# Kernel tuning notes

Measured on AMD Instinct MI355X. Metric: run time of the kernel, lower is better.

The kernel has to match this reference:

```python
import jax, jax.numpy as jnp
import numpy as np

N, E, D_IN, D, D_OUT, L = 50000, 800000, 128, 256, 64, 3
TAU0 = 0.5
LN_EPS = 1e-5


def setup_inputs() -> dict:
    key = jax.random.key(0)
    ks = jax.random.split(key, 16)
    u01 = jax.random.uniform(ks[2], (L, 2, N, 2), minval=1e-6, maxval=1.0 - 1e-6)
    gumbel = -jnp.log(-jnp.log(u01))  # standard Gumbel(0,1) noise, one draw per layer per action net
    s = lambda k, shape, fan: jax.random.normal(k, shape) * np.float32(1.0 / np.sqrt(fan))
    return {
        'x': jax.random.normal(ks[0], (N, D_IN), dtype=jnp.float32),
        'edge_index': jax.random.randint(ks[1], (2, E), 0, N),
        'gumbel_noise': gumbel,
        'W_enc': s(ks[3], (D_IN, D), D_IN), 'b_enc': jnp.zeros((D,), jnp.float32),
        'W_root': s(ks[4], (L, D, D), D), 'W_agg': s(ks[5], (L, D, D), D), 'b_env': jnp.zeros((L, D), jnp.float32),
        'Wa_in_r': s(ks[6], (D, 2), D), 'Wa_in_a': s(ks[7], (D, 2), D), 'b_in': jnp.zeros((2,), jnp.float32),
        'Wa_out_r': s(ks[8], (D, 2), D), 'Wa_out_a': s(ks[9], (D, 2), D), 'b_out': jnp.zeros((2,), jnp.float32),
        'Wt_r': s(ks[10], (D, 1), D), 'Wt_a': s(ks[11], (D, 1), D), 'b_t': jnp.zeros((1,), jnp.float32),
        'ln_g': jnp.ones((D,), jnp.float32), 'ln_b': jnp.zeros((D,), jnp.float32),
        'W_dec': s(ks[12], (D, D_OUT), D), 'b_dec': jnp.zeros((D_OUT,), jnp.float32),
    }


def reference(x, edge_index, gumbel_noise, W_enc, b_enc, W_root, W_agg, b_env,
              Wa_in_r, Wa_in_a, b_in, Wa_out_r, Wa_out_a, b_out,
              Wt_r, Wt_a, b_t, ln_g, ln_b, W_dec, b_dec):
    n = x.shape[0]
    u, v = edge_index[0], edge_index[1]  # message flows v -> u (aggregate at u)

    def conv(h, Wr, Wa, b, ew=None):
        # GraphConv-style: root transform + sum-aggregated (optionally edge-weighted) neighbor transform
        msg = h[v] if ew is None else ew[:, None] * h[v]  # [E, D]
        agg = jax.ops.segment_sum(msg, u, num_segments=n)  # [N, D]
        return h @ Wr + agg @ Wa + b

    def layernorm(h):
        m = jnp.mean(h, axis=-1, keepdims=True)
        var = jnp.mean((h - m) ** 2, axis=-1, keepdims=True)
        return (h - m) * jax.lax.rsqrt(var + LN_EPS) * ln_g + ln_b

    def gumbel_hard(logits, g, temp):
        # hard gumbel-softmax with straight-through estimator, per-node temperature
        y = jax.nn.softmax((logits + g) / temp, axis=-1)
        hard = jax.nn.one_hot(jnp.argmax(y, axis=-1), 2, dtype=y.dtype)
        return hard + y - jax.lax.stop_gradient(y)

    # env encoder + (dropout=identity) + relu
    h = jax.nn.relu(x @ W_enc + b_enc)

    for l in range(W_root.shape[0]):
        h = layernorm(h)
        in_logits = conv(h, Wa_in_r, Wa_in_a, b_in)    # [N, 2]
        out_logits = conv(h, Wa_out_r, Wa_out_a, b_out)  # [N, 2]
        t = conv(h, Wt_r, Wt_a, b_t)                   # [N, 1]
        temp = 1.0 / (jax.nn.softplus(t) + TAU0)       # TempSoftPlus: per-node inverse temperature
        in_prob = gumbel_hard(in_logits, gumbel_noise[l, 0], temp)
        out_prob = gumbel_hard(out_logits, gumbel_noise[l, 1], temp)
        ew = in_prob[:, 0][u] * out_prob[:, 0][v]      # [E] gated edge weights
        h = jax.nn.relu(conv(h, W_root[l], W_agg[l], b_env[l], ew))

    h = layernorm(h)
    return h @ W_dec + b_dec
```

## Files before the change

### kernel.cpp

```cpp
#include <hip/hip_runtime.h>
#include <cstdint>

#define NN 50000
#define EE 800000
#define DIN 128
#define DD 256
#define DOUT 64
#define NLAYERS 3
#define LN_EPS 1e-5f
#define NB_SCAN ((NN + 255) / 256)

typedef __attribute__((ext_vector_type(8))) unsigned short us8;
typedef __attribute__((ext_vector_type(8))) short bs8;
typedef __attribute__((ext_vector_type(4))) float f4;

__device__ __forceinline__ float waveSum(float v) {
#pragma unroll
  for (int m = 1; m < 64; m <<= 1) v += __shfl_xor(v, m, 64);
  return v;
}

__device__ __forceinline__ void split3(float a, unsigned short& s1, unsigned short& s2,
                                       unsigned short& s3) {
  unsigned int b = __float_as_uint(a);
  s1 = (unsigned short)(b >> 16);
  float r1 = a - __uint_as_float(b & 0xffff0000u);
  unsigned int c = __float_as_uint(r1);
  s2 = (unsigned short)(c >> 16);
  float r2 = r1 - __uint_as_float(c & 0xffff0000u);
  s3 = (unsigned short)(__float_as_uint(r2) >> 16);
}

__device__ __forceinline__ void split8(float4 a, float4 b, us8& l1, us8& l2, us8& l3) {
  unsigned short s1, s2, s3;
  split3(a.x, s1, s2, s3); l1[0] = s1; l2[0] = s2; l3[0] = s3;
  split3(a.y, s1, s2, s3); l1[1] = s1; l2[1] = s2; l3[1] = s3;
  split3(a.z, s1, s2, s3); l1[2] = s1; l2[2] = s2; l3[2] = s3;
  split3(a.w, s1, s2, s3); l1[3] = s1; l2[3] = s2; l3[3] = s3;
  split3(b.x, s1, s2, s3); l1[4] = s1; l2[4] = s2; l3[4] = s3;
  split3(b.y, s1, s2, s3); l1[5] = s1; l2[5] = s2; l3[5] = s3;
  split3(b.z, s1, s2, s3); l1[6] = s1; l2[6] = s2; l3[6] = s3;
  split3(b.w, s1, s2, s3); l1[7] = s1; l2[7] = s2; l3[7] = s3;
}

__global__ __launch_bounds__(256) void k_encoder(const float* __restrict__ x,
                                                 const float* __restrict__ W,
                                                 const float* __restrict__ b,
                                                 float* __restrict__ h) {
  __shared__ float xs[8][DIN];
  const int tid = threadIdx.x;
  const int row0 = blockIdx.x * 8;
  {
    int idx = tid * 4;
    int r = idx >> 7, c = idx & 127;
    int row = row0 + r;
    float4 v = make_float4(0.f, 0.f, 0.f, 0.f);
    if (row < NN) v = *(const float4*)(x + (size_t)row * DIN + c);
    *(float4*)(&xs[r][c]) = v;
  }
  __syncthreads();
  float acc[8] = {0.f, 0.f, 0.f, 0.f, 0.f, 0.f, 0.f, 0.f};
  const int d = tid;
#pragma unroll 8
  for (int k = 0; k < DIN; ++k) {
    float wk = W[(size_t)k * DD + d];
#pragma unroll
    for (int r = 0; r < 8; ++r) acc[r] = fmaf(xs[r][k], wk, acc[r]);
  }
  float bb = b[d];
#pragma unroll
  for (int r = 0; r < 8; ++r) {
    int row = row0 + r;
    if (row < NN) h[(size_t)row * DD + d] = fmaxf(acc[r] + bb, 0.f);
  }
}

__global__ __launch_bounds__(256) void k_ln_scalars(
    const float* __restrict__ h, const float* __restrict__ ln_g, const float* __restrict__ ln_b,
    const float* __restrict__ Wir, const float* __restrict__ Wia,
    const float* __restrict__ Wor, const float* __restrict__ Woa,
    float* __restrict__ hn, float* __restrict__ SR, float* __restrict__ SA) {
  const int lane = threadIdx.x & 63;
  const int node = blockIdx.x * 4 + (threadIdx.x >> 6);
  if (node >= NN) return;
  const float4 hv = *(const float4*)(h + (size_t)node * DD + lane * 4);
  float m = waveSum(hv.x + hv.y + hv.z + hv.w) * (1.f / DD);
  float dx = hv.x - m, dy = hv.y - m, dz = hv.z - m, dw = hv.w - m;
  float var = waveSum(dx * dx + dy * dy + dz * dz + dw * dw) * (1.f / DD);
  float rs = 1.f / sqrtf(var + LN_EPS);
  const float4 g = *(const float4*)(ln_g + lane * 4);
  const float4 bb = *(const float4*)(ln_b + lane * 4);
  float4 o;
  o.x = fmaf(dx * rs, g.x, bb.x);
  o.y = fmaf(dy * rs, g.y, bb.y);
  o.z = fmaf(dz * rs, g.z, bb.z);
  o.w = fmaf(dw * rs, g.w, bb.w);
  *(float4*)(hn + (size_t)node * DD + lane * 4) = o;
  float p[8];
  const float4 a0 = *(const float4*)(Wir + 8 * lane);
  const float4 a1 = *(const float4*)(Wir + 8 * lane + 4);
  p[0] = o.x * a0.x + o.y * a0.z + o.z * a1.x + o.w * a1.z;
  p[1] = o.x * a0.y + o.y * a0.w + o.z * a1.y + o.w * a1.w;
  const float4 c0 = *(const float4*)(Wia + 8 * lane);
  const float4 c1 = *(const float4*)(Wia + 8 * lane + 4);
  p[2] = o.x * c0.x + o.y * c0.z + o.z * c1.x + o.w * c1.z;
  p[3] = o.x * c0.y + o.y * c0.w + o.z * c1.y + o.w * c1.w;
  const float4 e0 = *(const float4*)(Wor + 8 * lane);
  const float4 e1 = *(const float4*)(Wor + 8 * lane + 4);
  p[4] = o.x * e0.x + o.y * e0.z + o.z * e1.x + o.w * e1.z;
  p[5] = o.x * e0.y + o.y * e0.w + o.z * e1.y + o.w * e1.w;
  const float4 f0 = *(const float4*)(Woa + 8 * lane);
  const float4 f1 = *(const float4*)(Woa + 8 * lane + 4);
  p[6] = o.x * f0.x + o.y * f0.z + o.z * f1.x + o.w * f1.z;
  p[7] = o.x * f0.y + o.y * f0.w + o.z * f1.y + o.w * f1.w;
#pragma unroll
  for (int j = 0; j < 8; ++j) p[j] = waveSum(p[j]);
  if (lane == 0) {
    *(float4*)(SR + (size_t)node * 4) = make_float4(p[0], p[1], p[4], p[5]);
    *(float4*)(SA + (size_t)node * 4) = make_float4(p[2], p[3], p[6], p[7]);
  }
}

__global__ void k_zero_deg(int* __restrict__ deg) {
  int i = blockIdx.x * 256 + threadIdx.x;
  if (i < NN) deg[i] = 0;
}

__global__ void k_deg(const int* __restrict__ ei, int* __restrict__ deg) {
  int e = blockIdx.x * 256 + threadIdx.x;
  if (e < EE) atomicAdd(&deg[ei[e]], 1);
}

__global__ __launch_bounds__(256) void k_scan1(const int* __restrict__ deg,
                                               int* __restrict__ bsum) {
  __shared__ int sm[256];
  const int t = threadIdx.x;
  int i = blockIdx.x * 256 + t;
  sm[t] = (i < NN) ? deg[i] : 0;
  __syncthreads();
  for (int off = 128; off > 0; off >>= 1) {
    if (t < off) sm[t] += sm[t + off];
    __syncthreads();
  }
  if (t == 0) bsum[blockIdx.x] = sm[0];
}

__global__ __launch_bounds__(256) void k_scan2(const int* __restrict__ bsum,
                                               int* __restrict__ boff,
                                               int* __restrict__ rowptr) {
  __shared__ int sm[256];
  const int t = threadIdx.x;
  int v = (t < NB_SCAN) ? bsum[t] : 0;
  sm[t] = v;
  __syncthreads();
  for (int off = 1; off < 256; off <<= 1) {
    int x = (t >= off) ? sm[t - off] : 0;
    __syncthreads();
    sm[t] += x;
    __syncthreads();
  }
  if (t < NB_SCAN) boff[t] = sm[t] - v;
  if (t == 0) rowptr[NN] = sm[255];
}

__global__ __launch_bounds__(256) void k_scan3(const int* __restrict__ deg,
                                               const int* __restrict__ boff,
                                               int* __restrict__ rowptr,
                                               int* __restrict__ cursor) {
  __shared__ int sm[256];
  const int t = threadIdx.x;
  int i = blockIdx.x * 256 + t;
  int v = (i < NN) ? deg[i] : 0;
  sm[t] = v;
  __syncthreads();
  for (int off = 1; off < 256; off <<= 1) {
    int x = (t >= off) ? sm[t - off] : 0;
    __syncthreads();
    sm[t] += x;
    __syncthreads();
  }
  if (i < NN) {
    int r = boff[blockIdx.x] + sm[t] - v;
    rowptr[i] = r;
    cursor[i] = r;
  }
}

__global__ void k_fill(const int* __restrict__ ei, int* __restrict__ cursor,
                       int* __restrict__ csr_v) {
  int e = blockIdx.x * 256 + threadIdx.x;
  if (e >= EE) return;
  int u = ei[e], v = ei[EE + e];
  int slot = atomicAdd(&cursor[u], 1);
  csr_v[slot] = v;
}

__global__ void k_prep_w3(const float* __restrict__ Wr, const float* __restrict__ Wa, int l,
                          unsigned short* __restrict__ W1, unsigned short* __restrict__ W2,
                          unsigned short* __restrict__ W3) {
  int idx = blockIdx.x * 256 + threadIdx.x;
  if (idx >= DD * 2 * DD) return;
  int n = idx >> 9;
  int k = idx & 511;
  float w = (k < DD) ? Wr[((size_t)l * DD + k) * DD + n]
                     : Wa[((size_t)l * DD + (k - DD)) * DD + n];
  unsigned short s1, s2, s3;
  split3(w, s1, s2, s3);
  W1[idx] = s1; W2[idx] = s2; W3[idx] = s3;
}

__global__ __launch_bounds__(256) void k_gates_csr(
    const int* __restrict__ rowptr, const int* __restrict__ csr_v,
    const float* __restrict__ SR, const float* __restrict__ SA,
    const float* __restrict__ gn, const float* __restrict__ b_in,
    const float* __restrict__ b_out, unsigned char* __restrict__ gin,
    unsigned char* __restrict__ gout, int l) {
  int u = blockIdx.x * 256 + threadIdx.x;
  if (u >= NN) return;
  int beg = rowptr[u], end = rowptr[u + 1];
  float4 a = make_float4(0.f, 0.f, 0.f, 0.f);
  for (int j = beg; j < end; ++j) {
    int v = csr_v[j];
    float4 s = *(const float4*)(SA + (size_t)v * 4);
    a.x += s.x; a.y += s.y; a.z += s.z; a.w += s.w;
  }
  float4 r = *(const float4*)(SR + (size_t)u * 4);
  const float* gi = gn + ((size_t)(l * 2 + 0) * NN + u) * 2;
  const float* go = gn + ((size_t)(l * 2 + 1) * NN + u) * 2;
  float li0 = r.x + a.x + b_in[0] + gi[0];
  float li1 = r.y + a.y + b_in[1] + gi[1];
  gin[u] = (li0 >= li1) ? 1 : 0;
  float lo0 = r.z + a.z + b_out[0] + go[0];
  float lo1 = r.w + a.w + b_out[1] + go[1];
  gout[u] = (lo0 >= lo1) ? 1 : 0;
}

__global__ __launch_bounds__(256) void k_wagg_csr(
    const int* __restrict__ rowptr, const int* __restrict__ csr_v,
    const unsigned char* __restrict__ gin, const unsigned char* __restrict__ gout,
    const float* __restrict__ hn, float* __restrict__ agg) {
  const int lane = threadIdx.x & 63;
  const int u = blockIdx.x * 4 + (threadIdx.x >> 6);
  if (u >= NN) return;
  float4 acc = make_float4(0.f, 0.f, 0.f, 0.f);
  float4 acc2 = make_float4(0.f, 0.f, 0.f, 0.f);
  if (gin[u]) {
    int beg = rowptr[u], end = rowptr[u + 1];
    for (int j0 = beg; j0 < end; j0 += 64) {
      int rem = end - j0;
      int v = -1;
      if (lane < rem) v = csr_v[j0 + lane];
      int ok = (v >= 0) ? (int)gout[v] : 0;
      unsigned long long mask = __ballot(ok);
      while (mask) {
        int l0 = __builtin_ctzll(mask);
        mask &= mask - 1;
        int vv0 = __shfl(v, l0);
        const float4* p0 = (const float4*)(hn + (size_t)vv0 * DD + lane * 4);
        if (mask) {
          int l1 = __builtin_ctzll(mask);
          mask &= mask - 1;
          int vv1 = __shfl(v, l1);
          const float4* p1 = (const float4*)(hn + (size_t)vv1 * DD + lane * 4);
          float4 h0 = *p0;
          float4 h1 = *p1;
          acc.x += h0.x; acc.y += h0.y; acc.z += h0.z; acc.w += h0.w;
          acc2.x += h1.x; acc2.y += h1.y; acc2.z += h1.z; acc2.w += h1.w;
        } else {
          float4 h0 = *p0;
          acc.x += h0.x; acc.y += h0.y; acc.z += h0.z; acc.w += h0.w;
        }
      }
    }
    acc.x += acc2.x; acc.y += acc2.y; acc.z += acc2.z; acc.w += acc2.w;
  }
  *(float4*)(agg + (size_t)u * DD + lane * 4) = acc;
}

#define BM 128
#define BN 128
#define LDP 40

__global__ __launch_bounds__(256, 2) void k_conv_mfma(
    const float* __restrict__ A0,
    const float* __restrict__ A1,
    const unsigned short* __restrict__ B1, const unsigned short* __restrict__ B2,
    const unsigned short* __restrict__ B3,
    const float* __restrict__ bias, float* __restrict__ hout) {
  __shared__ unsigned short lA1[BM * LDP], lA2[BM * LDP], lA3[BM * LDP];
  __shared__ unsigned short lB1[BN * LDP], lB2[BN * LDP], lB3[BN * LDP];
  const int tid = threadIdx.x;
  const int j0 = blockIdx.x * BN;
  const int i0 = blockIdx.y * BM;
  const int lane = tid & 63, w = tid >> 6;
  const int wr = w >> 1, wc = w & 1;
  const int fr = lane & 15, fs = (lane >> 4) * 8;
  const int srow = tid >> 1, sc0 = (tid & 1) * 16;
  int ga = i0 + srow;
  if (ga >= NN) ga = NN - 1;
  const size_t aoff = (size_t)ga * DD;
  const size_t boff = (size_t)(j0 + srow) * (2 * DD);
  const f4 fz = {0.f, 0.f, 0.f, 0.f};
  f4 acc[4][4];
#pragma unroll
  for (int i = 0; i < 4; ++i)
#pragma unroll
    for (int j = 0; j < 4; ++j) acc[i][j] = fz;

  float4 fa0, fa1, fa2, fa3;
  us8 rb1a, rb1b, rb2a, rb2b, rb3a, rb3b;
  {
    const float* pa = A0 + aoff + sc0;
    fa0 = *(const float4*)(pa);      fa1 = *(const float4*)(pa + 4);
    fa2 = *(const float4*)(pa + 8);  fa3 = *(const float4*)(pa + 12);
    rb1a = *(const us8*)(B1 + boff + sc0); rb1b = *(const us8*)(B1 + boff + sc0 + 8);
    rb2a = *(const us8*)(B2 + boff + sc0); rb2b = *(const us8*)(B2 + boff + sc0 + 8);
    rb3a = *(const us8*)(B3 + boff + sc0); rb3b = *(const us8*)(B3 + boff + sc0 + 8);
  }
  for (int kt = 0; kt < 16; ++kt) {
    __syncthreads();
    {
      int o = srow * LDP + sc0;
      us8 x1, x2, x3, y1, y2, y3;
      split8(fa0, fa1, x1, x2, x3);
      split8(fa2, fa3, y1, y2, y3);
      *(us8*)&lA1[o] = x1; *(us8*)&lA1[o + 8] = y1;
      *(us8*)&lA2[o] = x2; *(us8*)&lA2[o + 8] = y2;
      *(us8*)&lA3[o] = x3; *(us8*)&lA3[o + 8] = y3;
      *(us8*)&lB1[o] = rb1a; *(us8*)&lB1[o + 8] = rb1b;
      *(us8*)&lB2[o] = rb2a; *(us8*)&lB2[o + 8] = rb2b;
      *(us8*)&lB3[o] = rb3a; *(us8*)&lB3[o + 8] = rb3b;
    }
    __syncthreads();
    if (kt < 15) {
      int kb = (kt + 1) * 32;
      const float* abase = (kb < DD) ? A0 : A1;
      int kk = kb & (DD - 1);
      const float* pa = abase + aoff + kk + sc0;
      fa0 = *(const float4*)(pa);      fa1 = *(const float4*)(pa + 4);
      fa2 = *(const float4*)(pa + 8);  fa3 = *(const float4*)(pa + 12);
      rb1a = *(const us8*)(B1 + boff + kb + sc0); rb1b = *(const us8*)(B1 + boff + kb + sc0 + 8);
      rb2a = *(const us8*)(B2 + boff + kb + sc0); rb2b = *(const us8*)(B2 + boff + kb + sc0 + 8);
      rb3a = *(const us8*)(B3 + boff + kb + sc0); rb3b = *(const us8*)(B3 + boff + kb + sc0 + 8);
    }
    bs8 a1[4], a2[4], a3[4];
#pragma unroll
    for (int mi = 0; mi < 4; ++mi) {
      int r = (wr * 64 + mi * 16 + fr) * LDP + fs;
      a1[mi] = *(const bs8*)&lA1[r];
      a2[mi] = *(const bs8*)&lA2[r];
      a3[mi] = *(const bs8*)&lA3[r];
    }
#pragma unroll
    for (int ni = 0; ni < 4; ++ni) {
      int c = (wc * 64 + ni * 16 + fr) * LDP + fs;
      bs8 b1 = *(const bs8*)&lB1[c];
      bs8 b2 = *(const bs8*)&lB2[c];
      bs8 b3 = *(const bs8*)&lB3[c];
#pragma unroll
      for (int mi = 0; mi < 4; ++mi) {
        acc[mi][ni] = __builtin_amdgcn_mfma_f32_16x16x32_bf16(a1[mi], b1, acc[mi][ni], 0, 0, 0);
        acc[mi][ni] = __builtin_amdgcn_mfma_f32_16x16x32_bf16(a1[mi], b2, acc[mi][ni], 0, 0, 0);
        acc[mi][ni] = __builtin_amdgcn_mfma_f32_16x16x32_bf16(a2[mi], b1, acc[mi][ni], 0, 0, 0);
        acc[mi][ni] = __builtin_amdgcn_mfma_f32_16x16x32_bf16(a1[mi], b3, acc[mi][ni], 0, 0, 0);
        acc[mi][ni] = __builtin_amdgcn_mfma_f32_16x16x32_bf16(a2[mi], b2, acc[mi][ni], 0, 0, 0);
        acc[mi][ni] = __builtin_amdgcn_mfma_f32_16x16x32_bf16(a3[mi], b1, acc[mi][ni], 0, 0, 0);
      }
    }
  }
#pragma unroll
  for (int ni = 0; ni < 4; ++ni) {
    int col = j0 + wc * 64 + ni * 16 + fr;
    float bv = bias[col];
#pragma unroll
    for (int mi = 0; mi < 4; ++mi) {
      int rbase = i0 + wr * 64 + mi * 16 + (lane >> 4) * 4;
#pragma unroll
      for (int r = 0; r < 4; ++r) {
        int row = rbase + r;
        if (row < NN) hout[(size_t)row * DD + col] = fmaxf(acc[mi][ni][r] + bv, 0.f);
      }
    }
  }
}

__global__ __launch_bounds__(256) void k_dec(const float* __restrict__ hn,
                                             const float* __restrict__ Wd, const float* __restrict__ bd,
                                             float* __restrict__ out) {
  __shared__ float As[64][33];
  __shared__ float Bs[32][65];
  const int tid = threadIdx.x;
  const int i0 = blockIdx.x * 64;
  const int tx = tid & 15, ty = tid >> 4;
  const int arow = tid >> 2, acol = (tid & 3) * 8;
  const int brow = tid >> 3, bcol = (tid & 7) * 8;
  float acc[4][4] = {{0.f}};
  for (int k0 = 0; k0 < DD; k0 += 32) {
    {
      int gr = i0 + arow;
      if (gr >= NN) gr = NN - 1;
      const float* src = hn + (size_t)gr * DD + k0 + acol;
      *(float4*)(&As[arow][acol]) = *(const float4*)(src);
      *(float4*)(&As[arow][acol + 4]) = *(const float4*)(src + 4);
    }
    {
      const float* src = Wd + (size_t)(k0 + brow) * DOUT + bcol;
      *(float4*)(&Bs[brow][bcol]) = *(const float4*)(src);
      *(float4*)(&Bs[brow][bcol + 4]) = *(const float4*)(src + 4);
    }
    __syncthreads();
#pragma unroll
    for (int kk = 0; kk < 32; ++kk) {
      float av[4], bv[4];
#pragma unroll
      for (int r = 0; r < 4; ++r) av[r] = As[ty * 4 + r][kk];
#pragma unroll
      for (int c = 0; c < 4; ++c) bv[c] = Bs[kk][tx * 4 + c];
#pragma unroll
      for (int r = 0; r < 4; ++r)
#pragma unroll
        for (int c = 0; c < 4; ++c) acc[r][c] = fmaf(av[r], bv[c], acc[r][c]);
    }
    __syncthreads();
  }
  const float4 bj = *(const float4*)(bd + tx * 4);
#pragma unroll
  for (int r = 0; r < 4; ++r) {
    int gr = i0 + ty * 4 + r;
    if (gr < NN) {
      float4 o;
      o.x = acc[r][0] + bj.x;
      o.y = acc[r][1] + bj.y;
      o.z = acc[r][2] + bj.z;
      o.w = acc[r][3] + bj.w;
      *(float4*)(out + (size_t)gr * DOUT + tx * 4) = o;
    }
  }
}

extern "C" void kernel_launch(void* const* d_in, const int* in_sizes, int n_in,
                              void* d_out, int out_size, void* d_ws, size_t ws_size,
                              hipStream_t stream) {
  const float* x = (const float*)d_in[0];
  const int* ei = (const int*)d_in[1];
  const float* gn = (const float*)d_in[2];
  const float* W_enc = (const float*)d_in[3];
  const float* b_enc = (const float*)d_in[4];
  const float* W_root = (const float*)d_in[5];
  const float* W_agg = (const float*)d_in[6];
  const float* b_env = (const float*)d_in[7];
  const float* Wa_in_r = (const float*)d_in[8];
  const float* Wa_in_a = (const float*)d_in[9];
  const float* b_in = (const float*)d_in[10];
  const float* Wa_out_r = (const float*)d_in[11];
  const float* Wa_out_a = (const float*)d_in[12];
  const float* b_out = (const float*)d_in[13];
  const float* ln_g = (const float*)d_in[17];
  const float* ln_b = (const float*)d_in[18];
  const float* W_dec = (const float*)d_in[19];
  const float* b_dec = (const float*)d_in[20];
  float* out = (float*)d_out;

  float* ws = (float*)d_ws;
  size_t off = 0;
  float* h = ws + off;    off += (size_t)NN * DD;
  float* hn = ws + off;   off += (size_t)NN * DD;
  float* agg = ws + off;  off += (size_t)NN * DD;
  float* SR = ws + off;   off += (size_t)NN * 4;
  float* SA = ws + off;   off += (size_t)NN * 4;
  int* rowptr = (int*)(ws + off); off += (size_t)NN + 4;
  int* csr_v = (int*)(ws + off);  off += (size_t)EE;
  unsigned char* gin = (unsigned char*)(ws + off);  off += (size_t)NN / 4;
  unsigned char* gout = (unsigned char*)(ws + off); off += (size_t)NN / 4;
  unsigned short* WT1 = (unsigned short*)(ws + off); off += (size_t)DD * 2 * DD / 2;
  unsigned short* WT2 = (unsigned short*)(ws + off); off += (size_t)DD * 2 * DD / 2;
  unsigned short* WT3 = (unsigned short*)(ws + off); off += (size_t)DD * 2 * DD / 2;
  if (ws_size < off * sizeof(float)) return;
  int* deg = (int*)SR;
  int* bsum = (int*)SR + NN;
  int* boff = (int*)SR + NN + 256;
  int* cursor = (int*)SA;

  k_zero_deg<<<(NN + 255) / 256, 256, 0, stream>>>(deg);
  k_deg<<<(EE + 255) / 256, 256, 0, stream>>>(ei, deg);
  k_scan1<<<NB_SCAN, 256, 0, stream>>>(deg, bsum);
  k_scan2<<<1, 256, 0, stream>>>(bsum, boff, rowptr);
  k_scan3<<<NB_SCAN, 256, 0, stream>>>(deg, boff, rowptr, cursor);
  k_fill<<<(EE + 255) / 256, 256, 0, stream>>>(ei, cursor, csr_v);

  k_encoder<<<(NN + 7) / 8, 256, 0, stream>>>(x, W_enc, b_enc, h);

  for (int l = 0; l < NLAYERS; ++l) {
    k_ln_scalars<<<(NN + 3) / 4, 256, 0, stream>>>(h, ln_g, ln_b, Wa_in_r, Wa_in_a,
                                                   Wa_out_r, Wa_out_a, hn, SR, SA);
    k_gates_csr<<<(NN + 255) / 256, 256, 0, stream>>>(rowptr, csr_v, SR, SA, gn,
                                                      b_in, b_out, gin, gout, l);
    k_wagg_csr<<<(NN + 3) / 4, 256, 0, stream>>>(rowptr, csr_v, gin, gout, hn, agg);
    k_prep_w3<<<(DD * 2 * DD + 255) / 256, 256, 0, stream>>>(W_root, W_agg, l, WT1, WT2, WT3);
    k_conv_mfma<<<dim3(2, (NN + BM - 1) / BM), 256, 0, stream>>>(
        hn, agg, WT1, WT2, WT3, b_env + (size_t)l * DD, h);
  }

  k_ln_scalars<<<(NN + 3) / 4, 256, 0, stream>>>(h, ln_g, ln_b, Wa_in_r, Wa_in_a,
                                                 Wa_out_r, Wa_out_a, hn, SR, SA);
  k_dec<<<(NN + 63) / 64, 256, 0, stream>>>(hn, W_dec, b_dec, out);
}
```

Measured before the change: 919.2 us.

## Switch GEMMs to 2-term fp16 split MFMA and route encoder/decoder through it

Replaces the 3-way bf16 split (6 MFMAs per tile step) with a 2-way fp16 hi/lo split using 3 MFMAs, which halves the tensor-core work and the shared-memory traffic of the conv GEMM. The kernel becomes a template that is also used for the encoder and decoder GEMMs, replacing their scalar FP32 kernels. Launch bounds rise to 4 blocks per CU, since less shared memory is needed. The risk is precision: fp16 has a narrow exponent range, so very small residuals or large values may lose accuracy compared with the bf16 three-term scheme.

```diff
diff --git a/kernel.cpp b/kernel.cpp
--- a/kernel.cpp
+++ b/kernel.cpp
@@ -10,8 +10,7 @@
 #define LN_EPS 1e-5f
 #define NB_SCAN ((NN + 255) / 256)
 
-typedef __attribute__((ext_vector_type(8))) unsigned short us8;
-typedef __attribute__((ext_vector_type(8))) short bs8;
+typedef __attribute__((ext_vector_type(8))) _Float16 h8;
 typedef __attribute__((ext_vector_type(4))) float f4;
 
 __device__ __forceinline__ float waveSum(float v) {
@@ -20,58 +19,13 @@
   return v;
 }
 
-__device__ __forceinline__ void split3(float a, unsigned short& s1, unsigned short& s2,
-                                       unsigned short& s3) {
-  unsigned int b = __float_as_uint(a);
-  s1 = (unsigned short)(b >> 16);
-  float r1 = a - __uint_as_float(b & 0xffff0000u);
-  unsigned int c = __float_as_uint(r1);
-  s2 = (unsigned short)(c >> 16);
-  float r2 = r1 - __uint_as_float(c & 0xffff0000u);
-  s3 = (unsigned short)(__float_as_uint(r2) >> 16);
-}
-
-__device__ __forceinline__ void split8(float4 a, float4 b, us8& l1, us8& l2, us8& l3) {
-  unsigned short s1, s2, s3;
-  split3(a.x, s1, s2, s3); l1[0] = s1; l2[0] = s2; l3[0] = s3;
-  split3(a.y, s1, s2, s3); l1[1] = s1; l2[1] = s2; l3[1] = s3;
-  split3(a.z, s1, s2, s3); l1[2] = s1; l2[2] = s2; l3[2] = s3;
-  split3(a.w, s1, s2, s3); l1[3] = s1; l2[3] = s2; l3[3] = s3;
-  split3(b.x, s1, s2, s3); l1[4] = s1; l2[4] = s2; l3[4] = s3;
-  split3(b.y, s1, s2, s3); l1[5] = s1; l2[5] = s2; l3[5] = s3;
-  split3(b.z, s1, s2, s3); l1[6] = s1; l2[6] = s2; l3[6] = s3;
-  split3(b.w, s1, s2, s3); l1[7] = s1; l2[7] = s2; l3[7] = s3;
-}
-
-__global__ __launch_bounds__(256) void k_encoder(const float* __restrict__ x,
-                                                 const float* __restrict__ W,
-                                                 const float* __restrict__ b,
-                                                 float* __restrict__ h) {
-  __shared__ float xs[8][DIN];
-  const int tid = threadIdx.x;
-  const int row0 = blockIdx.x * 8;
-  {
-    int idx = tid * 4;
-    int r = idx >> 7, c = idx & 127;
-    int row = row0 + r;
-    float4 v = make_float4(0.f, 0.f, 0.f, 0.f);
-    if (row < NN) v = *(const float4*)(x + (size_t)row * DIN + c);
-    *(float4*)(&xs[r][c]) = v;
-  }
-  __syncthreads();
-  float acc[8] = {0.f, 0.f, 0.f, 0.f, 0.f, 0.f, 0.f, 0.f};
-  const int d = tid;
-#pragma unroll 8
-  for (int k = 0; k < DIN; ++k) {
-    float wk = W[(size_t)k * DD + d];
-#pragma unroll
-    for (int r = 0; r < 8; ++r) acc[r] = fmaf(xs[r][k], wk, acc[r]);
-  }
-  float bb = b[d];
-#pragma unroll
-  for (int r = 0; r < 8; ++r) {
-    int row = row0 + r;
-    if (row < NN) h[(size_t)row * DD + d] = fmaxf(acc[r] + bb, 0.f);
+__device__ __forceinline__ void splith(const float4& a, const float4& b, h8& p1, h8& p2) {
+  float t[8] = {a.x, a.y, a.z, a.w, b.x, b.y, b.z, b.w};
+#pragma unroll
+  for (int i = 0; i < 8; ++i) {
+    _Float16 x = (_Float16)t[i];
+    p1[i] = x;
+    p2[i] = (_Float16)(t[i] - (float)x);
   }
 }
 
@@ -195,18 +149,27 @@
   csr_v[slot] = v;
 }
 
-__global__ void k_prep_w3(const float* __restrict__ Wr, const float* __restrict__ Wa, int l,
-                          unsigned short* __restrict__ W1, unsigned short* __restrict__ W2,
-                          unsigned short* __restrict__ W3) {
+__global__ void k_prep_generic(const float* __restrict__ W, int K, int N,
+                               _Float16* __restrict__ W1, _Float16* __restrict__ W2) {
+  int idx = blockIdx.x * 256 + threadIdx.x;
+  if (idx >= K * N) return;
+  int n = idx / K, k = idx - n * K;
+  float w = W[(size_t)k * N + n];
+  _Float16 x = (_Float16)w;
+  W1[idx] = x;
+  W2[idx] = (_Float16)(w - (float)x);
+}
+
+__global__ void k_prep_conv(const float* __restrict__ Wr, const float* __restrict__ Wa, int l,
+                            _Float16* __restrict__ W1, _Float16* __restrict__ W2) {
   int idx = blockIdx.x * 256 + threadIdx.x;
   if (idx >= DD * 2 * DD) return;
-  int n = idx >> 9;
-  int k = idx & 511;
+  int n = idx >> 9, k = idx & 511;
   float w = (k < DD) ? Wr[((size_t)l * DD + k) * DD + n]
                      : Wa[((size_t)l * DD + (k - DD)) * DD + n];
-  unsigned short s1, s2, s3;
-  split3(w, s1, s2, s3);
-  W1[idx] = s1; W2[idx] = s2; W3[idx] = s3;
+  _Float16 x = (_Float16)w;
+  W1[idx] = x;
+  W2[idx] = (_Float16)(w - (float)x);
 }
 
 __global__ __launch_bounds__(256) void k_gates_csr(
@@ -278,99 +241,110 @@
 }
 
 #define BM 128
-#define BN 128
 #define LDP 40
 
-__global__ __launch_bounds__(256, 2) void k_conv_mfma(
-    const float* __restrict__ A0,
-    const float* __restrict__ A1,
-    const unsigned short* __restrict__ B1, const unsigned short* __restrict__ B2,
-    const unsigned short* __restrict__ B3,
-    const float* __restrict__ bias, float* __restrict__ hout) {
-  __shared__ unsigned short lA1[BM * LDP], lA2[BM * LDP], lA3[BM * LDP];
-  __shared__ unsigned short lB1[BN * LDP], lB2[BN * LDP], lB3[BN * LDP];
+template <int KTOT, int ASTR, int NFN, int OSTR, bool RELU, bool DUAL>
+__global__ __launch_bounds__(256, 4) void k_mfma_gemm(
+    const float* __restrict__ A0, const float* __restrict__ A1,
+    const _Float16* __restrict__ B1, const _Float16* __restrict__ B2,
+    const float* __restrict__ bias, float* __restrict__ outp) {
+  constexpr int BN = NFN * 32;
+  constexpr int KSTEPS = KTOT / 32;
+  __shared__ _Float16 lA1[BM * LDP], lA2[BM * LDP];
+  __shared__ _Float16 lB1[BN * LDP], lB2[BN * LDP];
   const int tid = threadIdx.x;
   const int j0 = blockIdx.x * BN;
   const int i0 = blockIdx.y * BM;
   const int lane = tid & 63, w = tid >> 6;
   const int wr = w >> 1, wc = w & 1;
   const int fr = lane & 15, fs = (lane >> 4) * 8;
-  const int srow = tid >> 1, sc0 = (tid & 1) * 16;
-  int ga = i0 + srow;
+  const int asr = tid >> 1, asc = (tid & 1) * 16;
+  int ga = i0 + asr;
   if (ga >= NN) ga = NN - 1;
-  const size_t aoff = (size_t)ga * DD;
-  const size_t boff = (size_t)(j0 + srow) * (2 * DD);
-  const f4 fz = {0.f, 0.f, 0.f, 0.f};
-  f4 acc[4][4];
+  const int bsr = (BN == 128) ? (tid >> 1) : (tid >> 2);
+  const int bsc = (BN == 128) ? ((tid & 1) * 16) : ((tid & 3) * 8);
+  const size_t boff = (size_t)(j0 + bsr) * KTOT + bsc;
+
+  f4 acc[4][NFN];
 #pragma unroll
   for (int i = 0; i < 4; ++i)
 #pragma unroll
-    for (int j = 0; j < 4; ++j) acc[i][j] = fz;
+    for (int j = 0; j < NFN; ++j) acc[i][j] = (f4){0.f, 0.f, 0.f, 0.f};
 
   float4 fa0, fa1, fa2, fa3;
-  us8 rb1a, rb1b, rb2a, rb2b, rb3a, rb3b;
+  h8 rb1a, rb1b, rb2a, rb2b;
   {
-    const float* pa = A0 + aoff + sc0;
-    fa0 = *(const float4*)(pa);      fa1 = *(const float4*)(pa + 4);
-    fa2 = *(const float4*)(pa + 8);  fa3 = *(const float4*)(pa + 12);
-    rb1a = *(const us8*)(B1 + boff + sc0); rb1b = *(const us8*)(B1 + boff + sc0 + 8);
-    rb2a = *(const us8*)(B2 + boff + sc0); rb2b = *(const us8*)(B2 + boff + sc0 + 8);
-    rb3a = *(const us8*)(B3 + boff + sc0); rb3b = *(const us8*)(B3 + boff + sc0 + 8);
-  }
-  for (int kt = 0; kt < 16; ++kt) {
+    const float* pa;
+    if constexpr (DUAL) pa = A0 + (size_t)ga * DD + asc;
+    else pa = A0 + (size_t)ga * ASTR + asc;
+    fa0 = *(const float4*)(pa);     fa1 = *(const float4*)(pa + 4);
+    fa2 = *(const float4*)(pa + 8); fa3 = *(const float4*)(pa + 12);
+    rb1a = *(const h8*)(B1 + boff);
+    rb2a = *(const h8*)(B2 + boff);
+    if constexpr (BN == 128) {
+      rb1b = *(const h8*)(B1 + boff + 8);
+      rb2b = *(const h8*)(B2 + boff + 8);
+    }
+  }
+  for (int kt = 0; kt < KSTEPS; ++kt) {
     __syncthreads();
     {
-      int o = srow * LDP + sc0;
-      us8 x1, x2, x3, y1, y2, y3;
-      split8(fa0, fa1, x1, x2, x3);
-      split8(fa2, fa3, y1, y2, y3);
-      *(us8*)&lA1[o] = x1; *(us8*)&lA1[o + 8] = y1;
-      *(us8*)&lA2[o] = x2; *(us8*)&lA2[o + 8] = y2;
-      *(us8*)&lA3[o] = x3; *(us8*)&lA3[o + 8] = y3;
-      *(us8*)&lB1[o] = rb1a; *(us8*)&lB1[o + 8] = rb1b;
-      *(us8*)&lB2[o] = rb2a; *(us8*)&lB2[o + 8] = rb2b;
-      *(us8*)&lB3[o] = rb3a; *(us8*)&lB3[o + 8] = rb3b;
-    }
-    __syncthreads();
-    if (kt < 15) {
+      int o = asr * LDP + asc;
+      h8 p1a, p1b, p2a, p2b;
+      splith(fa0, fa1, p1a, p2a);
+      splith(fa2, fa3, p1b, p2b);
+      *(h8*)&lA1[o] = p1a; *(h8*)&lA1[o + 8] = p1b;
+      *(h8*)&lA2[o] = p2a; *(h8*)&lA2[o + 8] = p2b;
+      int ob = bsr * LDP + bsc;
+      *(h8*)&lB1[ob] = rb1a;
+      *(h8*)&lB2[ob] = rb2a;
+      if constexpr (BN == 128) {
+        *(h8*)&lB1[ob + 8] = rb1b;
+        *(h8*)&lB2[ob + 8] = rb2b;
+      }
+    }
+    __syncthreads();
+    if (kt < KSTEPS - 1) {
       int kb = (kt + 1) * 32;
-      const float* abase = (kb < DD) ? A0 : A1;
-      int kk = kb & (DD - 1);
-      const float* pa = abase + aoff + kk + sc0;
-      fa0 = *(const float4*)(pa);      fa1 = *(const float4*)(pa + 4);
-      fa2 = *(const float4*)(pa + 8);  fa3 = *(const float4*)(pa + 12);
-      rb1a = *(const us8*)(B1 + boff + kb + sc0); rb1b = *(const us8*)(B1 + boff + kb + sc0 + 8);
-      rb2a = *(const us8*)(B2 + boff + kb + sc0); rb2b = *(const us8*)(B2 + boff + kb + sc0 + 8);
-      rb3a = *(const us8*)(B3 + boff + kb + sc0); rb3b = *(const us8*)(B3 + boff + kb + sc0 + 8);
-    }
-    bs8 a1[4], a2[4], a3[4];
+      const float* pa;
+      if constexpr (DUAL) {
+        const float* ab = (kb < DD) ? A0 : A1;
+        pa = ab + (size_t)ga * DD + (kb & (DD - 1)) + asc;
+      } else {
+        pa = A0 + (size_t)ga * ASTR + kb + asc;
+      }
+      fa0 = *(const float4*)(pa);     fa1 = *(const float4*)(pa + 4);
+      fa2 = *(const float4*)(pa + 8); fa3 = *(const float4*)(pa + 12);
+      rb1a = *(const h8*)(B1 + boff + kb);
+      rb2a = *(const h8*)(B2 + boff + kb);
+      if constexpr (BN == 128) {
+        rb1b = *(const h8*)(B1 + boff + kb + 8);
+        rb2b = *(const h8*)(B2 + boff + kb + 8);
+      }
+    }
+    h8 a1[4], a2[4];
 #pragma unroll
     for (int mi = 0; mi < 4; ++mi) {
       int r = (wr * 64 + mi * 16 + fr) * LDP + fs;
-      a1[mi] = *(const bs8*)&lA1[r];
-      a2[mi] = *(const bs8*)&lA2[r];
-      a3[mi] = *(const bs8*)&lA3[r];
-    }
-#pragma unroll
-    for (int ni = 0; ni < 4; ++ni) {
-      int c = (wc * 64 + ni * 16 + fr) * LDP + fs;
-      bs8 b1 = *(const bs8*)&lB1[c];
-      bs8 b2 = *(const bs8*)&lB2[c];
-      bs8 b3 = *(const bs8*)&lB3[c];
+      a1[mi] = *(const h8*)&lA1[r];
+      a2[mi] = *(const h8*)&lA2[r];
+    }
+#pragma unroll
+    for (int ni = 0; ni < NFN; ++ni) {
+      int c = (wc * (NFN * 16) + ni * 16 + fr) * LDP + fs;
+      h8 b1 = *(const h8*)&lB1[c];
+      h8 b2 = *(const h8*)&lB2[c];
 #pragma unroll
       for (int mi = 0; mi < 4; ++mi) {
-        acc[mi][ni] = __builtin_amdgcn_mfma_f32_16x16x32_bf16(a1[mi], b1, acc[mi][ni], 0, 0, 0);
-        acc[mi][ni] = __builtin_amdgcn_mfma_f32_16x16x32_bf16(a1[mi], b2, acc[mi][ni], 0, 0, 0);
-        acc[mi][ni] = __builtin_amdgcn_mfma_f32_16x16x32_bf16(a2[mi], b1, acc[mi][ni], 0, 0, 0);
-        acc[mi][ni] = __builtin_amdgcn_mfma_f32_16x16x32_bf16(a1[mi], b3, acc[mi][ni], 0, 0, 0);
-        acc[mi][ni] = __builtin_amdgcn_mfma_f32_16x16x32_bf16(a2[mi], b2, acc[mi][ni], 0, 0, 0);
-        acc[mi][ni] = __builtin_amdgcn_mfma_f32_16x16x32_bf16(a3[mi], b1, acc[mi][ni], 0, 0, 0);
-      }
-    }
-  }
-#pragma unroll
-  for (int ni = 0; ni < 4; ++ni) {
-    int col = j0 + wc * 64 + ni * 16 + fr;
+        acc[mi][ni] = __builtin_amdgcn_mfma_f32_16x16x32_f16(a1[mi], b1, acc[mi][ni], 0, 0, 0);
+        acc[mi][ni] = __builtin_amdgcn_mfma_f32_16x16x32_f16(a1[mi], b2, acc[mi][ni], 0, 0, 0);
+        acc[mi][ni] = __builtin_amdgcn_mfma_f32_16x16x32_f16(a2[mi], b1, acc[mi][ni], 0, 0, 0);
+      }
+    }
+  }
+#pragma unroll
+  for (int ni = 0; ni < NFN; ++ni) {
+    int col = j0 + wc * (NFN * 16) + ni * 16 + fr;
     float bv = bias[col];
 #pragma unroll
     for (int mi = 0; mi < 4; ++mi) {
@@ -378,62 +352,11 @@
 #pragma unroll
       for (int r = 0; r < 4; ++r) {
         int row = rbase + r;
-        if (row < NN) hout[(size_t)row * DD + col] = fmaxf(acc[mi][ni][r] + bv, 0.f);
-      }
-    }
-  }
-}
-
-__global__ __launch_bounds__(256) void k_dec(const float* __restrict__ hn,
-                                             const float* __restrict__ Wd, const float* __restrict__ bd,
-                                             float* __restrict__ out) {
-  __shared__ float As[64][33];
-  __shared__ float Bs[32][65];
-  const int tid = threadIdx.x;
-  const int i0 = blockIdx.x * 64;
-  const int tx = tid & 15, ty = tid >> 4;
-  const int arow = tid >> 2, acol = (tid & 3) * 8;
-  const int brow = tid >> 3, bcol = (tid & 7) * 8;
-  float acc[4][4] = {{0.f}};
-  for (int k0 = 0; k0 < DD; k0 += 32) {
-    {
-      int gr = i0 + arow;
-      if (gr >= NN) gr = NN - 1;
-      const float* src = hn + (size_t)gr * DD + k0 + acol;
-      *(float4*)(&As[arow][acol]) = *(const float4*)(src);
-      *(float4*)(&As[arow][acol + 4]) = *(const float4*)(src + 4);
-    }
-    {
-      const float* src = Wd + (size_t)(k0 + brow) * DOUT + bcol;
-      *(float4*)(&Bs[brow][bcol]) = *(const float4*)(src);
-      *(float4*)(&Bs[brow][bcol + 4]) = *(const float4*)(src + 4);
-    }
-    __syncthreads();
-#pragma unroll
-    for (int kk = 0; kk < 32; ++kk) {
-      float av[4], bv[4];
-#pragma unroll
-      for (int r = 0; r < 4; ++r) av[r] = As[ty * 4 + r][kk];
-#pragma unroll
-      for (int c = 0; c < 4; ++c) bv[c] = Bs[kk][tx * 4 + c];
-#pragma unroll
-      for (int r = 0; r < 4; ++r)
-#pragma unroll
-        for (int c = 0; c < 4; ++c) acc[r][c] = fmaf(av[r], bv[c], acc[r][c]);
-    }
-    __syncthreads();
-  }
-  const float4 bj = *(const float4*)(bd + tx * 4);
-#pragma unroll
-  for (int r = 0; r < 4; ++r) {
-    int gr = i0 + ty * 4 + r;
-    if (gr < NN) {
-      float4 o;
-      o.x = acc[r][0] + bj.x;
-      o.y = acc[r][1] + bj.y;
-      o.z = acc[r][2] + bj.z;
-      o.w = acc[r][3] + bj.w;
-      *(float4*)(out + (size_t)gr * DOUT + tx * 4) = o;
+        if (row < NN) {
+          float v = acc[mi][ni][r] + bv;
+          outp[(size_t)row * OSTR + col] = RELU ? fmaxf(v, 0.f) : v;
+        }
+      }
     }
   }
 }
@@ -472,9 +395,12 @@
   int* csr_v = (int*)(ws + off);  off += (size_t)EE;
   unsigned char* gin = (unsigned char*)(ws + off);  off += (size_t)NN / 4;
   unsigned char* gout = (unsigned char*)(ws + off); off += (size_t)NN / 4;
-  unsigned short* WT1 = (unsigned short*)(ws + off); off += (size_t)DD * 2 * DD / 2;
-  unsigned short* WT2 = (unsigned short*)(ws + off); off += (size_t)DD * 2 * DD / 2;
-  unsigned short* WT3 = (unsigned short*)(ws + off); off += (size_t)DD * 2 * DD / 2;
+  _Float16* cW1 = (_Float16*)(ws + off); off += (size_t)DD * 2 * DD / 2;
+  _Float16* cW2 = (_Float16*)(ws + off); off += (size_t)DD * 2 * DD / 2;
+  _Float16* eW1 = (_Float16*)(ws + off); off += (size_t)DD * DIN / 2;
+  _Float16* eW2 = (_Float16*)(ws + off); off += (size_t)DD * DIN / 2;
+  _Float16* dW1 = (_Float16*)(ws + off); off += (size_t)DOUT * DD / 2;
+  _Float16* dW2 = (_Float16*)(ws + off); off += (size_t)DOUT * DD / 2;
   if (ws_size < off * sizeof(float)) return;
   int* deg = (int*)SR;
   int* bsum = (int*)SR + NN;
@@ -488,7 +414,12 @@
   k_scan3<<<NB_SCAN, 256, 0, stream>>>(deg, boff, rowptr, cursor);
   k_fill<<<(EE + 255) / 256, 256, 0, stream>>>(ei, cursor, csr_v);
 
-  k_encoder<<<(NN + 7) / 8, 256, 0, stream>>>(x, W_enc, b_enc, h);
+  k_prep_generic<<<(DIN * DD + 255) / 256, 256, 0, stream>>>(W_enc, DIN, DD, eW1, eW2);
+  k_prep_generic<<<(DD * DOUT + 255) / 256, 256, 0, stream>>>(W_dec, DD, DOUT, dW1, dW2);
+
+  const int gy = (NN + BM - 1) / BM;
+  k_mfma_gemm<DIN, DIN, 4, DD, true, false><<<dim3(2, gy), 256, 0, stream>>>(
+      x, nullptr, eW1, eW2, b_enc, h);
 
   for (int l = 0; l < NLAYERS; ++l) {
     k_ln_scalars<<<(NN + 3) / 4, 256, 0, stream>>>(h, ln_g, ln_b, Wa_in_r, Wa_in_a,
@@ -496,12 +427,13 @@
     k_gates_csr<<<(NN + 255) / 256, 256, 0, stream>>>(rowptr, csr_v, SR, SA, gn,
                                                       b_in, b_out, gin, gout, l);
     k_wagg_csr<<<(NN + 3) / 4, 256, 0, stream>>>(rowptr, csr_v, gin, gout, hn, agg);
-    k_prep_w3<<<(DD * 2 * DD + 255) / 256, 256, 0, stream>>>(W_root, W_agg, l, WT1, WT2, WT3);
-    k_conv_mfma<<<dim3(2, (NN + BM - 1) / BM), 256, 0, stream>>>(
-        hn, agg, WT1, WT2, WT3, b_env + (size_t)l * DD, h);
+    k_prep_conv<<<(DD * 2 * DD + 255) / 256, 256, 0, stream>>>(W_root, W_agg, l, cW1, cW2);
+    k_mfma_gemm<2 * DD, DD, 4, DD, true, true><<<dim3(2, gy), 256, 0, stream>>>(
+        hn, agg, cW1, cW2, b_env + (size_t)l * DD, h);
   }
 
   k_ln_scalars<<<(NN + 3) / 4, 256, 0, stream>>>(h, ln_g, ln_b, Wa_in_r, Wa_in_a,
                                                  Wa_out_r, Wa_out_a, hn, SR, SA);
-  k_dec<<<(NN + 63) / 64, 256, 0, stream>>>(hn, W_dec, b_dec, out);
-}
+  k_mfma_gemm<DD, DD, 2, DOUT, false, false><<<dim3(1, gy), 256, 0, stream>>>(
+      hn, nullptr, dW1, dW2, b_dec, out);
+}
```

New measurement: 737.5 us. 19.8% less time.
